# Performance work log

Hardware: AMD Instinct MI355X
Metric: run time of the kernel (lower is better)

The kernel has to match this reference:

```python
import jax, jax.numpy as jnp
import numpy as np

K = 9
BN_EPS = 1e-5
NEG_SLOPE = 0.2


def setup_inputs() -> dict:
    key = jax.random.key(0)
    ks = jax.random.split(key, 8)
    B, C, H, W = 16, 128, 32, 32
    s1 = 1.0 / np.sqrt(2 * C)
    s2 = 1.0 / np.sqrt(C)
    return {
        "x": jax.random.normal(ks[0], (B, C, H, W), dtype=jnp.float32),
        "W1": jax.random.uniform(ks[1], (2 * C, C), dtype=jnp.float32, minval=-s1, maxval=s1),
        "b1": jax.random.uniform(ks[2], (C,), dtype=jnp.float32, minval=-s1, maxval=s1),
        "W2": jax.random.uniform(ks[3], (C, C), dtype=jnp.float32, minval=-s2, maxval=s2),
        "b2": jax.random.uniform(ks[4], (C,), dtype=jnp.float32, minval=-s2, maxval=s2),
        "gamma": jnp.ones((C,), dtype=jnp.float32),
        "beta": jnp.zeros((C,), dtype=jnp.float32),
    }


def _leaky_relu(h):
    return jnp.where(h >= 0, h, NEG_SLOPE * h)


def reference(x, W1, b1, W2, b2, gamma, beta):
    B, C, H, W = x.shape
    N = H * W
    r = x
    feats = x.reshape(B, C, N).transpose(0, 2, 1)  # (B, N, C)

    # pairwise squared Euclidean distances (ordering identical to torch.cdist p=2)
    sq = jnp.sum(feats * feats, axis=-1)  # (B, N)
    d2 = sq[:, :, None] + sq[:, None, :] - 2.0 * jnp.einsum("bnc,bmc->bnm", feats, feats)
    _, idx = jax.lax.top_k(-d2, K)  # k smallest distances -> (B, N, K) int32

    neighbors = jax.vmap(lambda f, i: f[i])(feats, idx)  # (B, N, K, C)
    center = feats[:, :, None, :]  # (B, N, 1, C)
    edge = jnp.concatenate(
        [jnp.broadcast_to(center, neighbors.shape), neighbors - center], axis=-1
    )  # (B, N, K, 2C)

    h = _leaky_relu(edge @ W1 + b1)
    h = h @ W2 + b2  # (B, N, K, C)
    msg = jnp.max(h, axis=2)  # (B, N, C)

    out = msg.transpose(0, 2, 1).reshape(B, C, H, W)

    # BatchNorm2d (training mode: batch statistics, biased variance)
    mean = jnp.mean(out, axis=(0, 2, 3), keepdims=True)
    var = jnp.mean((out - mean) ** 2, axis=(0, 2, 3), keepdims=True)
    g = gamma.reshape(1, C, 1, 1)
    b = beta.reshape(1, C, 1, 1)
    out = g * (out - mean) * jax.lax.rsqrt(var + BN_EPS) + b

    return jax.nn.relu(out + r)
```

## Files before the change

### kernel.cpp

```cpp
#include <hip/hip_runtime.h>

#define B_ 16
#define C_ 128
#define N_ 1024
#define K_ 9
#define NEG_SLOPE 0.2f
#define BN_EPS 1e-5f

typedef __attribute__((ext_vector_type(8))) short short8;
typedef __attribute__((ext_vector_type(4))) float f32x4;
typedef __attribute__((ext_vector_type(4))) unsigned short u16x4;

__device__ __forceinline__ unsigned short f2bf(float f) {
    union { float f; unsigned u; } v; v.f = f;
    unsigned r = v.u + 0x7fffu + ((v.u >> 16) & 1u);
    return (unsigned short)(r >> 16);
}
__device__ __forceinline__ float bf2f(unsigned short h) {
    union { unsigned u; float f; } v; v.u = ((unsigned)h) << 16; return v.f;
}
__device__ __forceinline__ unsigned umin_(unsigned a, unsigned b) { return a < b ? a : b; }

__global__ __launch_bounds__(256) void k_stage(const float* __restrict__ x,
        const float* __restrict__ W1, const float* __restrict__ W2,
        float* __restrict__ featsT, unsigned short* __restrict__ Bf,
        float* __restrict__ sq, unsigned short* __restrict__ wf1,
        unsigned short* __restrict__ wf2)
{
    int blk = blockIdx.x;
    int tid = threadIdx.x;

    if (blk >= 512) {
        int t = (blk - 512) * 256 + tid;
        if (t < 4096) {
            int kk = t >> 9, w = (t >> 6) & 7, lane = t & 63;
            int quad = lane >> 4, col = lane & 15;
            #pragma unroll
            for (int j = 0; j < 8; ++j)
                wf1[t * 8 + j] = f2bf(W1[(kk * 32 + quad * 8 + j) * C_ + 16 * w + col]);
        } else {
            int t2 = t - 4096;
            int kk = t2 >> 9, w = (t2 >> 6) & 7, lane = t2 & 63;
            int quad = lane >> 4, col = lane & 15;
            #pragma unroll
            for (int j = 0; j < 8; ++j)
                wf2[t2 * 8 + j] = f2bf(W2[(kk * 32 + quad * 8 + j) * C_ + 16 * w + col]);
        }
        return;
    }

    __shared__ float tch[128][33];
    int b = blk >> 5;
    int n0 = (blk & 31) * 32;

    const float4* xv = (const float4*)x;
    #pragma unroll
    for (int pass = 0; pass < 4; ++pass) {
        int c = pass * 32 + (tid >> 3);
        int f = tid & 7;
        float4 v = xv[(b * C_ + c) * 256 + (n0 >> 2) + f];
        tch[c][f * 4 + 0] = v.x; tch[c][f * 4 + 1] = v.y;
        tch[c][f * 4 + 2] = v.z; tch[c][f * 4 + 3] = v.w;
    }
    __syncthreads();

    #pragma unroll
    for (int pass = 0; pass < 16; ++pass) {
        int li = pass * 256 + tid;
        int p = li >> 7, c = li & 127;
        featsT[(b * N_ + n0 + p) * C_ + c] = tch[c][p];
    }

    int lane = tid & 63, wv = tid >> 6;
    int half = lane >> 5, l2 = lane & 31;
    int ch0 = (l2 & 15) * 8;
    #pragma unroll
    for (int sub = 0; sub < 4; ++sub) {
        int pl = sub * 8 + wv * 2 + half;
        int n = n0 + pl;
        float a0 = tch[ch0 + 0][pl], a1 = tch[ch0 + 1][pl];
        float a2 = tch[ch0 + 2][pl], a3 = tch[ch0 + 3][pl];
        float a4 = tch[ch0 + 4][pl], a5 = tch[ch0 + 5][pl];
        float a6 = tch[ch0 + 6][pl], a7 = tch[ch0 + 7][pl];

        u16x4 o0, o1;
        if (l2 < 16) {
            o0.x = f2bf(a0); o0.y = f2bf(a1); o0.z = f2bf(a2); o0.w = f2bf(a3);
            o1.x = f2bf(a4); o1.y = f2bf(a5); o1.z = f2bf(a6); o1.w = f2bf(a7);
        } else {
            o0.x = f2bf(a0 - bf2f(f2bf(a0))); o0.y = f2bf(a1 - bf2f(f2bf(a1)));
            o0.z = f2bf(a2 - bf2f(f2bf(a2))); o0.w = f2bf(a3 - bf2f(f2bf(a3)));
            o1.x = f2bf(a4 - bf2f(f2bf(a4))); o1.y = f2bf(a5 - bf2f(f2bf(a5)));
            o1.z = f2bf(a6 - bf2f(f2bf(a6))); o1.w = f2bf(a7 - bf2f(f2bf(a7)));
        }
        long chunk = (((long)(b * 8 + (l2 >> 2)) * 64 + (n >> 4)) << 6)
                   + ((l2 & 3) * 16 + (n & 15));
        *(u16x4*)&Bf[chunk * 8]     = o0;
        *(u16x4*)&Bf[chunk * 8 + 4] = o1;

        float ss = a0*a0 + a1*a1 + a2*a2 + a3*a3 + a4*a4 + a5*a5 + a6*a6 + a7*a7;
        #pragma unroll
        for (int off = 1; off < 16; off <<= 1)
            ss += __shfl_xor(ss, off);
        if (l2 == 0) sq[b * N_ + n] = ss;
    }
}

#define STAGE_READ(PH, VARR) do {                                              \
    const int tl_ = (PH) >> 1, rb_ = ((PH) & 1) * 2;                           \
    _Pragma("unroll")                                                          \
    for (int t = 0; t < 8; ++t) {                                              \
        int col = ((wv * 8 + t) << 4) + cl;                                    \
        keybuf[quad * 2 + 0][col] = karr[tl_][t][rb_ + 0];                     \
        keybuf[quad * 2 + 1][col] = karr[tl_][t][rb_ + 1];                     \
    }                                                                          \
    __syncthreads();                                                           \
    _Pragma("unroll")                                                          \
    for (int j = 0; j < 16; ++j) VARR[j] = keybuf[wv][lane + (j << 6)];        \
    __syncthreads();                                                           \
} while (0)

#define TOP2_INIT(VARR, M1, M2, J1, J2) do {                                   \
    M1 = 0xFFFFFFFFu; M2 = 0xFFFFFFFFu; J1 = 0; J2 = 0;                        \
    _Pragma("unroll")                                                          \
    for (int j = 0; j < 16; ++j) {                                             \
        unsigned x_ = VARR[j], jc_ = (unsigned)j;                              \
        bool b1_ = x_ < M1, b2_ = x_ < M2;                                     \
        unsigned tk_ = b1_ ? M1 : x_, tj_ = b1_ ? J1 : jc_;                    \
        M2 = b2_ ? tk_ : M2; J2 = b2_ ? tj_ : J2;                              \
        M1 = b1_ ? x_ : M1; J1 = b1_ ? jc_ : J1;                               \
    }                                                                          \
} while (0)

#define ROW_ROUND(VARR, M1, M2, J1, J2, G, ROWPTR) do {                        \
    bool t_ = (M1 == (G));                                                     \
    unsigned long long bal_ = __ballot(t_);                                    \
    bool win_;                                                                 \
    if (__popcll(bal_) > 1) {               \
        unsigned mc_ = t_ ? (unsigned)(lane + (J1 << 6)) : 0xFFFFFFFFu;        \
        unsigned cm_ = mc_;                                                    \
        _Pragma("unroll")                                                      \
        for (int off = 1; off < 64; off <<= 1)                                 \
            cm_ = umin_(cm_, (unsigned)__shfl_xor((int)cm_, off));             \
        win_ = t_ && (mc_ == cm_);                   \
    } else {                                                                   \
        win_ = t_;                                                             \
    }                                                                          \
    if (win_) {                                                                \
        idxout[(ROWPTR) + q] = lane + (int)(J1 << 6);                          \
        unsigned gk_ = M1, gj_ = J1;                                           \
        M1 = M2; J1 = J2; M2 = 0xFFFFFFFFu;                                    \
        if (M1 == 0xFFFFFFFFu) {             \
            _Pragma("unroll")                                                  \
            for (int j = 0; j < 16; ++j) {                                     \
                unsigned x_ = VARR[j], jc_ = (unsigned)j;                      \
                bool dead_ = (x_ < gk_) || (x_ == gk_ && jc_ <= gj_);          \
                unsigned xk_ = dead_ ? 0xFFFFFFFFu : x_;                       \
                bool b1_ = xk_ < M1, b2_ = xk_ < M2;                           \
                unsigned tk_ = b1_ ? M1 : xk_, tj_ = b1_ ? J1 : jc_;           \
                M2 = b2_ ? tk_ : M2; J2 = b2_ ? tj_ : J2;                      \
                M1 = b1_ ? xk_ : M1; J1 = b1_ ? jc_ : J1;                      \
            }                                                                  \
        }                                                                      \
    }                                                                          \
} while (0)

__global__ __launch_bounds__(512, 4) void k_knn(
        const unsigned short* __restrict__ Bf, const float* __restrict__ sq,
        int* __restrict__ idxout)
{
    __shared__ unsigned keybuf[8][1028];
    __shared__ float sqn[32];

    int L = blockIdx.x;
    int xcd = L & 7, slot = L >> 3;
    int b = xcd * 2 + (slot >> 5);
    int tile32 = slot & 31;
    int n0 = tile32 * 32;
    int tid = threadIdx.x;

    if (tid < 32) sqn[tid] = sq[b * N_ + n0 + tid];
    __syncthreads();

    int wv = tid >> 6, lane = tid & 63, quad = lane >> 4, cl = lane & 15;

    f32x4 acc[2][8];
    #pragma unroll
    for (int tl = 0; tl < 2; ++tl)
        #pragma unroll
        for (int t = 0; t < 8; ++t) acc[tl][t] = (f32x4){0.f, 0.f, 0.f, 0.f};

    const short8* bfp = (const short8*)Bf;
    #pragma unroll
    for (int kb = 0; kb < 4; ++kb) {
        long ab0 = (((long)(b * 8 + kb) * 64 + tile32 * 2) << 6) + quad * 16 + cl;
        short8 afh0 = bfp[ab0];
        short8 afl0 = bfp[ab0 + 16384];
        short8 afh1 = bfp[ab0 + 64];
        short8 afl1 = bfp[ab0 + 16384 + 64];
        long bh = (((long)(b * 8 + kb) * 64 + wv * 8) << 6) + lane;
        long bl = bh + 16384;
        #pragma unroll
        for (int t = 0; t < 8; ++t) {
            short8 bfr = bfp[bh + t * 64];
            acc[0][t] = __builtin_amdgcn_mfma_f32_16x16x32_bf16(afh0, bfr, acc[0][t], 0, 0, 0);
            acc[0][t] = __builtin_amdgcn_mfma_f32_16x16x32_bf16(afl0, bfr, acc[0][t], 0, 0, 0);
            acc[1][t] = __builtin_amdgcn_mfma_f32_16x16x32_bf16(afh1, bfr, acc[1][t], 0, 0, 0);
            acc[1][t] = __builtin_amdgcn_mfma_f32_16x16x32_bf16(afl1, bfr, acc[1][t], 0, 0, 0);
        }
        #pragma unroll
        for (int t = 0; t < 8; ++t) {
            short8 bfr = bfp[bl + t * 64];
            acc[0][t] = __builtin_amdgcn_mfma_f32_16x16x32_bf16(afh0, bfr, acc[0][t], 0, 0, 0);
            acc[1][t] = __builtin_amdgcn_mfma_f32_16x16x32_bf16(afh1, bfr, acc[1][t], 0, 0, 0);
        }
    }

    float smc[8];
    #pragma unroll
    for (int t = 0; t < 8; ++t)
        smc[t] = sq[b * N_ + ((wv * 8 + t) << 4) + cl];

    unsigned karr[2][8][4];
    #pragma unroll
    for (int tl = 0; tl < 2; ++tl)
        #pragma unroll
        for (int t = 0; t < 8; ++t)
            #pragma unroll
            for (int r = 0; r < 4; ++r) {
                float d2 = fmaf(-2.f, acc[tl][t][r], smc[t] + sqn[tl * 16 + quad * 4 + r]);
                unsigned bits = __float_as_uint(d2);
                karr[tl][t][r] = bits ^ ((unsigned)((int)bits >> 31) | 0x80000000u);
            }

    unsigned vA[16], vB[16], vC[16], vD[16];
    STAGE_READ(0, vA);
    STAGE_READ(1, vB);
    STAGE_READ(2, vC);
    STAGE_READ(3, vD);

    int rbase = ((wv >> 1) << 2) + (wv & 1);
    int rowP0 = (b * N_ + n0 + rbase) * K_;
    int rowP1 = (b * N_ + n0 + rbase + 2) * K_;
    int rowP2 = (b * N_ + n0 + 16 + rbase) * K_;
    int rowP3 = (b * N_ + n0 + 16 + rbase + 2) * K_;

    unsigned mA1, mA2, jA1, jA2, mB1, mB2, jB1, jB2;
    unsigned mC1, mC2, jC1, jC2, mD1, mD2, jD1, jD2;
    TOP2_INIT(vA, mA1, mA2, jA1, jA2);
    TOP2_INIT(vB, mB1, mB2, jB1, jB2);
    TOP2_INIT(vC, mC1, mC2, jC1, jC2);
    TOP2_INIT(vD, mD1, mD2, jD1, jD2);

    #pragma unroll 1
    for (int q = 0; q < K_; ++q) {
        unsigned gA = mA1, gB = mB1, gC = mC1, gD = mD1;
        #pragma unroll
        for (int off = 1; off < 64; off <<= 1) {
            gA = umin_(gA, (unsigned)__shfl_xor((int)gA, off));
            gB = umin_(gB, (unsigned)__shfl_xor((int)gB, off));
            gC = umin_(gC, (unsigned)__shfl_xor((int)gC, off));
            gD = umin_(gD, (unsigned)__shfl_xor((int)gD, off));
        }
        ROW_ROUND(vA, mA1, mA2, jA1, jA2, gA, rowP0);
        ROW_ROUND(vB, mB1, mB2, jB1, jB2, gB, rowP1);
        ROW_ROUND(vC, mC1, mC2, jC1, jC2, gC, rowP2);
        ROW_ROUND(vD, mD1, mD2, jD1, jD2, gD, rowP3);
    }
}

__global__ __launch_bounds__(512, 6) void k_edge(const float* __restrict__ featsT,
        const int* __restrict__ idx, const unsigned short* __restrict__ wf1,
        const unsigned short* __restrict__ wf2, const float* __restrict__ b1,
        const float* __restrict__ b2, float* __restrict__ msg)
{
    __shared__ __align__(16) char smem[52224];
    unsigned short* diffs = (unsigned short*)smem;
    unsigned short* cenb  = (unsigned short*)(smem + 21760);
    unsigned short* h2b   = (unsigned short*)smem;
    unsigned short* h1    = (unsigned short*)(smem + 26112);
    unsigned short* ccb   = (unsigned short*)(smem + 47872);
    __shared__ int nb[72];

    int L = blockIdx.x;
    int xcd = L & 7, slot = L >> 3;
    int b = xcd * 2 + (slot >> 7);
    int tile = slot & 127;
    int n0 = tile * 8;
    int tid = threadIdx.x;

    if (tid < 72) nb[tid] = idx[(b * N_ + n0 + tid / 9) * K_ + tid % 9];
    __syncthreads();

    {
        int g = tid >> 6, j = tid & 63;
        int chunk = j & 31, ch = chunk << 2, half = j >> 5;
        const float4* fT4 = (const float4*)featsT;
        float4 cv = fT4[(b * N_ + n0 + g) * 32 + chunk];
        if (half == 0) {
            u16x4 cb; cb.x = f2bf(cv.x); cb.y = f2bf(cv.y);
            cb.z = f2bf(cv.z); cb.w = f2bf(cv.w);
            *(u16x4*)&cenb[g * 136 + ch] = cb;
        }
        int qb = half ? 5 : 0, qe = half ? 9 : 5;
        for (int q = qb; q < qe; ++q) {
            int e = g * 9 + q;
            float4 nv = fT4[(b * N_ + nb[e]) * 32 + chunk];
            u16x4 db;
            db.x = f2bf(nv.x - cv.x); db.y = f2bf(nv.y - cv.y);
            db.z = f2bf(nv.z - cv.z); db.w = f2bf(nv.w - cv.w);
            *(u16x4*)&diffs[e * 136 + ch] = db;
        }
    }
    __syncthreads();

    int wv = tid >> 6, lane = tid & 63;
    int quad = lane >> 4, cl = lane & 15;
    const short8* w1f = (const short8*)wf1;
    const short8* w2f = (const short8*)wf2;

    {
        float b1v = b1[16 * wv + cl];
        f32x4 a = (f32x4){b1v, b1v, b1v, b1v};
        #pragma unroll
        for (int kk = 0; kk < 4; ++kk) {
            short8 af = *(const short8*)&cenb[cl * 136 + kk * 32 + quad * 8];
            short8 bf = w1f[(kk * 8 + wv) * 64 + lane];
            a = __builtin_amdgcn_mfma_f32_16x16x32_bf16(af, bf, a, 0, 0, 0);
        }
        #pragma unroll
        for (int r = 0; r < 4; ++r)
            ccb[(quad * 4 + r) * 136 + 16 * wv + cl] = f2bf(a[r]);
    }

    {
        short8 wb[4];
        #pragma unroll
        for (int kb = 0; kb < 4; ++kb)
            wb[kb] = w1f[((kb + 4) * 8 + wv) * 64 + lane];
        #pragma unroll
        for (int t = 0; t < 5; ++t) {
            f32x4 a = (f32x4){0.f, 0.f, 0.f, 0.f};
            #pragma unroll
            for (int kb = 0; kb < 4; ++kb) {
                short8 af = *(const short8*)&diffs[(16 * t + cl) * 136 + kb * 32 + quad * 8];
                a = __builtin_amdgcn_mfma_f32_16x16x32_bf16(af, wb[kb], a, 0, 0, 0);
            }
            #pragma unroll
            for (int r = 0; r < 4; ++r) {
                int row = 16 * t + quad * 4 + r;
                int pt = row / 9; if (pt > 7) pt = 7;
                float v = a[r] + bf2f(ccb[pt * 136 + 16 * wv + cl]);
                v = (v >= 0.f) ? v : NEG_SLOPE * v;
                h1[row * 136 + 16 * wv + cl] = f2bf(v);
            }
        }
    }
    __syncthreads();

    {
        short8 wb[4];
        #pragma unroll
        for (int kb = 0; kb < 4; ++kb)
            wb[kb] = w2f[(kb * 8 + wv) * 64 + lane];
        #pragma unroll
        for (int t = 0; t < 5; ++t) {
            f32x4 a = (f32x4){0.f, 0.f, 0.f, 0.f};
            #pragma unroll
            for (int kb = 0; kb < 4; ++kb) {
                short8 af = *(const short8*)&h1[(16 * t + cl) * 136 + kb * 32 + quad * 8];
                a = __builtin_amdgcn_mfma_f32_16x16x32_bf16(af, wb[kb], a, 0, 0, 0);
            }
            #pragma unroll
            for (int r = 0; r < 4; ++r)
                h2b[(16 * t + quad * 4 + r) * 136 + 16 * wv + cl] = f2bf(a[r]);
        }
    }
    __syncthreads();

    int p = tid & 7, nb8 = tid >> 3;
    #pragma unroll
    for (int it = 0; it < 2; ++it) {
        int n = nb8 + 64 * it;
        float m = bf2f(h2b[(p * 9) * 136 + n]);
        #pragma unroll
        for (int q = 1; q < 9; ++q)
            m = fmaxf(m, bf2f(h2b[(p * 9 + q) * 136 + n]));
        msg[(b * C_ + n) * N_ + n0 + p] = m + b2[n];
    }
}

__global__ __launch_bounds__(256) void k_bnstats(const float* __restrict__ msg,
        const float* __restrict__ gamma, const float* __restrict__ beta,
        float* __restrict__ scale, float* __restrict__ shift)
{
    int c = blockIdx.x, tid = threadIdx.x;
    const float4* m4 = (const float4*)msg;
    float4 s4 = {0.f, 0.f, 0.f, 0.f}, ss4 = {0.f, 0.f, 0.f, 0.f};
    #pragma unroll
    for (int b = 0; b < B_; ++b) {
        float4 v = m4[(b * C_ + c) * 256 + tid];
        s4.x += v.x; s4.y += v.y; s4.z += v.z; s4.w += v.w;
        ss4.x += v.x * v.x; ss4.y += v.y * v.y;
        ss4.z += v.z * v.z; ss4.w += v.w * v.w;
    }
    float s = (s4.x + s4.y) + (s4.z + s4.w);
    float ss = (ss4.x + ss4.y) + (ss4.z + ss4.w);
    __shared__ float rs[256], rss[256];
    rs[tid] = s; rss[tid] = ss;
    __syncthreads();
    for (int off = 128; off > 0; off >>= 1) {
        if (tid < off) { rs[tid] += rs[tid + off]; rss[tid] += rss[tid + off]; }
        __syncthreads();
    }
    if (tid == 0) {
        float mean = rs[0] / (float)(B_ * N_);
        float var = rss[0] / (float)(B_ * N_) - mean * mean;
        float inv = 1.0f / sqrtf(var + BN_EPS);
        float g = gamma[c];
        scale[c] = g * inv;
        shift[c] = beta[c] - g * inv * mean;
    }
}

__global__ __launch_bounds__(256) void k_final(const float* __restrict__ msg,
        const float* __restrict__ x, const float* __restrict__ scale,
        const float* __restrict__ shift, float* __restrict__ out)
{
    int i = blockIdx.x * 256 + threadIdx.x;
    int e = i << 2;
    int c = (e >> 10) & 127;
    float sc = scale[c], sh = shift[c];
    float4 m4 = reinterpret_cast<const float4*>(msg)[i];
    float4 x4 = reinterpret_cast<const float4*>(x)[i];
    float4 o;
    o.x = fmaxf(m4.x * sc + sh + x4.x, 0.f);
    o.y = fmaxf(m4.y * sc + sh + x4.y, 0.f);
    o.z = fmaxf(m4.z * sc + sh + x4.z, 0.f);
    o.w = fmaxf(m4.w * sc + sh + x4.w, 0.f);
    reinterpret_cast<float4*>(out)[i] = o;
}

extern "C" void kernel_launch(void* const* d_in, const int* in_sizes, int n_in,
                              void* d_out, int out_size, void* d_ws, size_t ws_size,
                              hipStream_t stream)
{
    const float* x     = (const float*)d_in[0];
    const float* W1    = (const float*)d_in[1];
    const float* b1    = (const float*)d_in[2];
    const float* W2    = (const float*)d_in[3];
    const float* b2    = (const float*)d_in[4];
    const float* gamma = (const float*)d_in[5];
    const float* beta  = (const float*)d_in[6];
    float* out = (float*)d_out;

    float* ws     = (float*)d_ws;
    float* featsT = ws;
    float* msg    = ws + 2097152;
    unsigned short* Bf = (unsigned short*)(ws + 2097152);
    float* sq     = ws + 4194304;
    float* scale  = ws + 4210688;
    float* shift  = ws + 4210816;
    int*   idx    = (int*)(ws + 4210944);
    unsigned short* wf1 = (unsigned short*)(ws + 4358400);
    unsigned short* wf2 = (unsigned short*)(ws + 4374784);

    k_stage  <<< 536, 256, 0, stream>>>(x, W1, W2, featsT, Bf, sq, wf1, wf2);
    k_knn    <<< 512, 512, 0, stream>>>(Bf, sq, idx);
    k_edge   <<<2048, 512, 0, stream>>>(featsT, idx, wf1, wf2, b1, b2, msg);
    k_bnstats<<< 128, 256, 0, stream>>>(msg, gamma, beta, scale, shift);
    k_final  <<<2048, 256, 0, stream>>>(msg, x, scale, shift, out);
}
```

Baseline: 142.0 us.

## Halve kNN row tile to 16 and split each row's top-k across half-waves

The kNN kernel now processes 16 query rows per block instead of 32, doubling the grid to 1024 blocks. Each half-wavefront (32 lanes) owns one query row, holding 32 candidate keys per lane instead of a full wavefront handling four rows with 16 keys per lane. The change aims for more parallelism and shorter dependent shuffle chains in the selection loop, with one row per thread group instead of four interleaved rows. In exchange each block reloads the full B operand for only 16 rows, roughly doubling redundant global/L2 traffic, and register pressure per thread rises.

```diff
diff --git a/kernel.cpp b/kernel.cpp
--- a/kernel.cpp
+++ b/kernel.cpp
@@ -106,113 +106,47 @@
     }
 }
 
-#define STAGE_READ(PH, VARR) do {                                              \
-    const int tl_ = (PH) >> 1, rb_ = ((PH) & 1) * 2;                           \
-    _Pragma("unroll")                                                          \
-    for (int t = 0; t < 8; ++t) {                                              \
-        int col = ((wv * 8 + t) << 4) + cl;                                    \
-        keybuf[quad * 2 + 0][col] = karr[tl_][t][rb_ + 0];                     \
-        keybuf[quad * 2 + 1][col] = karr[tl_][t][rb_ + 1];                     \
-    }                                                                          \
-    __syncthreads();                                                           \
-    _Pragma("unroll")                                                          \
-    for (int j = 0; j < 16; ++j) VARR[j] = keybuf[wv][lane + (j << 6)];        \
-    __syncthreads();                                                           \
-} while (0)
-
-#define TOP2_INIT(VARR, M1, M2, J1, J2) do {                                   \
-    M1 = 0xFFFFFFFFu; M2 = 0xFFFFFFFFu; J1 = 0; J2 = 0;                        \
-    _Pragma("unroll")                                                          \
-    for (int j = 0; j < 16; ++j) {                                             \
-        unsigned x_ = VARR[j], jc_ = (unsigned)j;                              \
-        bool b1_ = x_ < M1, b2_ = x_ < M2;                                     \
-        unsigned tk_ = b1_ ? M1 : x_, tj_ = b1_ ? J1 : jc_;                    \
-        M2 = b2_ ? tk_ : M2; J2 = b2_ ? tj_ : J2;                              \
-        M1 = b1_ ? x_ : M1; J1 = b1_ ? jc_ : J1;                               \
-    }                                                                          \
-} while (0)
-
-#define ROW_ROUND(VARR, M1, M2, J1, J2, G, ROWPTR) do {                        \
-    bool t_ = (M1 == (G));                                                     \
-    unsigned long long bal_ = __ballot(t_);                                    \
-    bool win_;                                                                 \
-    if (__popcll(bal_) > 1) {               \
-        unsigned mc_ = t_ ? (unsigned)(lane + (J1 << 6)) : 0xFFFFFFFFu;        \
-        unsigned cm_ = mc_;                                                    \
-        _Pragma("unroll")                                                      \
-        for (int off = 1; off < 64; off <<= 1)                                 \
-            cm_ = umin_(cm_, (unsigned)__shfl_xor((int)cm_, off));             \
-        win_ = t_ && (mc_ == cm_);                   \
-    } else {                                                                   \
-        win_ = t_;                                                             \
-    }                                                                          \
-    if (win_) {                                                                \
-        idxout[(ROWPTR) + q] = lane + (int)(J1 << 6);                          \
-        unsigned gk_ = M1, gj_ = J1;                                           \
-        M1 = M2; J1 = J2; M2 = 0xFFFFFFFFu;                                    \
-        if (M1 == 0xFFFFFFFFu) {             \
-            _Pragma("unroll")                                                  \
-            for (int j = 0; j < 16; ++j) {                                     \
-                unsigned x_ = VARR[j], jc_ = (unsigned)j;                      \
-                bool dead_ = (x_ < gk_) || (x_ == gk_ && jc_ <= gj_);          \
-                unsigned xk_ = dead_ ? 0xFFFFFFFFu : x_;                       \
-                bool b1_ = xk_ < M1, b2_ = xk_ < M2;                           \
-                unsigned tk_ = b1_ ? M1 : xk_, tj_ = b1_ ? J1 : jc_;           \
-                M2 = b2_ ? tk_ : M2; J2 = b2_ ? tj_ : J2;                      \
-                M1 = b1_ ? xk_ : M1; J1 = b1_ ? jc_ : J1;                      \
-            }                                                                  \
-        }                                                                      \
-    }                                                                          \
-} while (0)
-
 __global__ __launch_bounds__(512, 4) void k_knn(
         const unsigned short* __restrict__ Bf, const float* __restrict__ sq,
         int* __restrict__ idxout)
 {
-    __shared__ unsigned keybuf[8][1028];
-    __shared__ float sqn[32];
+    __shared__ unsigned keybuf[8][1032];
+    __shared__ float sqn[16];
 
     int L = blockIdx.x;
     int xcd = L & 7, slot = L >> 3;
-    int b = xcd * 2 + (slot >> 5);
-    int tile32 = slot & 31;
-    int n0 = tile32 * 32;
+    int b = xcd * 2 + (slot >> 6);
+    int tile = slot & 63;
+    int n0 = tile * 16;
     int tid = threadIdx.x;
 
-    if (tid < 32) sqn[tid] = sq[b * N_ + n0 + tid];
+    if (tid < 16) sqn[tid] = sq[b * N_ + n0 + tid];
     __syncthreads();
 
     int wv = tid >> 6, lane = tid & 63, quad = lane >> 4, cl = lane & 15;
 
-    f32x4 acc[2][8];
-    #pragma unroll
-    for (int tl = 0; tl < 2; ++tl)
-        #pragma unroll
-        for (int t = 0; t < 8; ++t) acc[tl][t] = (f32x4){0.f, 0.f, 0.f, 0.f};
+    f32x4 acc[8];
+    #pragma unroll
+    for (int t = 0; t < 8; ++t) acc[t] = (f32x4){0.f, 0.f, 0.f, 0.f};
 
     const short8* bfp = (const short8*)Bf;
     #pragma unroll
     for (int kb = 0; kb < 4; ++kb) {
-        long ab0 = (((long)(b * 8 + kb) * 64 + tile32 * 2) << 6) + quad * 16 + cl;
-        short8 afh0 = bfp[ab0];
-        short8 afl0 = bfp[ab0 + 16384];
-        short8 afh1 = bfp[ab0 + 64];
-        short8 afl1 = bfp[ab0 + 16384 + 64];
+        long abase = (((long)(b * 8 + kb) * 64 + tile) << 6) + quad * 16 + cl;
+        short8 afh = bfp[abase];
+        short8 afl = bfp[abase + 16384];
         long bh = (((long)(b * 8 + kb) * 64 + wv * 8) << 6) + lane;
         long bl = bh + 16384;
         #pragma unroll
         for (int t = 0; t < 8; ++t) {
             short8 bfr = bfp[bh + t * 64];
-            acc[0][t] = __builtin_amdgcn_mfma_f32_16x16x32_bf16(afh0, bfr, acc[0][t], 0, 0, 0);
-            acc[0][t] = __builtin_amdgcn_mfma_f32_16x16x32_bf16(afl0, bfr, acc[0][t], 0, 0, 0);
-            acc[1][t] = __builtin_amdgcn_mfma_f32_16x16x32_bf16(afh1, bfr, acc[1][t], 0, 0, 0);
-            acc[1][t] = __builtin_amdgcn_mfma_f32_16x16x32_bf16(afl1, bfr, acc[1][t], 0, 0, 0);
+            acc[t] = __builtin_amdgcn_mfma_f32_16x16x32_bf16(afh, bfr, acc[t], 0, 0, 0);
+            acc[t] = __builtin_amdgcn_mfma_f32_16x16x32_bf16(afl, bfr, acc[t], 0, 0, 0);
         }
         #pragma unroll
         for (int t = 0; t < 8; ++t) {
             short8 bfr = bfp[bl + t * 64];
-            acc[0][t] = __builtin_amdgcn_mfma_f32_16x16x32_bf16(afh0, bfr, acc[0][t], 0, 0, 0);
-            acc[1][t] = __builtin_amdgcn_mfma_f32_16x16x32_bf16(afh1, bfr, acc[1][t], 0, 0, 0);
+            acc[t] = __builtin_amdgcn_mfma_f32_16x16x32_bf16(afh, bfr, acc[t], 0, 0, 0);
         }
     }
 
@@ -221,51 +155,88 @@
     for (int t = 0; t < 8; ++t)
         smc[t] = sq[b * N_ + ((wv * 8 + t) << 4) + cl];
 
-    unsigned karr[2][8][4];
-    #pragma unroll
-    for (int tl = 0; tl < 2; ++tl)
-        #pragma unroll
-        for (int t = 0; t < 8; ++t)
-            #pragma unroll
-            for (int r = 0; r < 4; ++r) {
-                float d2 = fmaf(-2.f, acc[tl][t][r], smc[t] + sqn[tl * 16 + quad * 4 + r]);
-                unsigned bits = __float_as_uint(d2);
-                karr[tl][t][r] = bits ^ ((unsigned)((int)bits >> 31) | 0x80000000u);
-            }
-
-    unsigned vA[16], vB[16], vC[16], vD[16];
-    STAGE_READ(0, vA);
-    STAGE_READ(1, vB);
-    STAGE_READ(2, vC);
-    STAGE_READ(3, vD);
-
-    int rbase = ((wv >> 1) << 2) + (wv & 1);
-    int rowP0 = (b * N_ + n0 + rbase) * K_;
-    int rowP1 = (b * N_ + n0 + rbase + 2) * K_;
-    int rowP2 = (b * N_ + n0 + 16 + rbase) * K_;
-    int rowP3 = (b * N_ + n0 + 16 + rbase + 2) * K_;
-
-    unsigned mA1, mA2, jA1, jA2, mB1, mB2, jB1, jB2;
-    unsigned mC1, mC2, jC1, jC2, mD1, mD2, jD1, jD2;
-    TOP2_INIT(vA, mA1, mA2, jA1, jA2);
-    TOP2_INIT(vB, mB1, mB2, jB1, jB2);
-    TOP2_INIT(vC, mC1, mC2, jC1, jC2);
-    TOP2_INIT(vD, mD1, mD2, jD1, jD2);
+    unsigned karr[8][4];
+    #pragma unroll
+    for (int t = 0; t < 8; ++t)
+        #pragma unroll
+        for (int r = 0; r < 4; ++r) {
+            float d2 = fmaf(-2.f, acc[t][r], smc[t] + sqn[quad * 4 + r]);
+            unsigned bits = __float_as_uint(d2);
+            karr[t][r] = bits ^ ((unsigned)((int)bits >> 31) | 0x80000000u);
+        }
+
+    int grp = lane >> 5, l32 = lane & 31;
+    int myphase = wv >> 2;
+    int kr_r = ((wv & 3) << 1) + grp;
+    unsigned v[32];
+    #pragma unroll
+    for (int ph = 0; ph < 2; ++ph) {
+        #pragma unroll
+        for (int t = 0; t < 8; ++t) {
+            int col = ((wv * 8 + t) << 4) + cl;
+            keybuf[quad * 2 + 0][col] = karr[t][ph * 2 + 0];
+            keybuf[quad * 2 + 1][col] = karr[t][ph * 2 + 1];
+        }
+        __syncthreads();
+        if (myphase == ph) {
+            #pragma unroll
+            for (int j = 0; j < 32; ++j)
+                v[j] = keybuf[kr_r][(j << 5) + l32];
+        }
+        __syncthreads();
+    }
+
+    int rowq = ((kr_r >> 1) << 2) + (myphase << 1) + (kr_r & 1);
+    long orow = (long)(b * N_ + n0 + rowq) * K_;
+
+    unsigned m1 = 0xFFFFFFFFu, m2 = 0xFFFFFFFFu, j1 = 0, j2 = 0;
+    #pragma unroll
+    for (int j = 0; j < 32; ++j) {
+        unsigned x_ = v[j], jc = (unsigned)j;
+        bool b1 = x_ < m1, b2 = x_ < m2;
+        unsigned tk = b1 ? m1 : x_, tj = b1 ? j1 : jc;
+        m2 = b2 ? tk : m2; j2 = b2 ? tj : j2;
+        m1 = b1 ? x_ : m1; j1 = b1 ? jc : j1;
+    }
 
     #pragma unroll 1
     for (int q = 0; q < K_; ++q) {
-        unsigned gA = mA1, gB = mB1, gC = mC1, gD = mD1;
-        #pragma unroll
-        for (int off = 1; off < 64; off <<= 1) {
-            gA = umin_(gA, (unsigned)__shfl_xor((int)gA, off));
-            gB = umin_(gB, (unsigned)__shfl_xor((int)gB, off));
-            gC = umin_(gC, (unsigned)__shfl_xor((int)gC, off));
-            gD = umin_(gD, (unsigned)__shfl_xor((int)gD, off));
-        }
-        ROW_ROUND(vA, mA1, mA2, jA1, jA2, gA, rowP0);
-        ROW_ROUND(vB, mB1, mB2, jB1, jB2, gB, rowP1);
-        ROW_ROUND(vC, mC1, mC2, jC1, jC2, gC, rowP2);
-        ROW_ROUND(vD, mD1, mD2, jD1, jD2, gD, rowP3);
+        unsigned g = m1;
+        #pragma unroll
+        for (int off = 1; off < 32; off <<= 1)
+            g = umin_(g, (unsigned)__shfl_xor((int)g, off));
+
+        bool tied = (m1 == g);
+        unsigned long long bal = __ballot(tied);
+        unsigned balg = (unsigned)(bal >> (grp << 5));
+        bool win;
+        if (__popc(balg) > 1) {
+            unsigned mc = tied ? ((j1 << 5) + (unsigned)l32) : 0xFFFFFFFFu;
+            unsigned cm = mc;
+            #pragma unroll
+            for (int off = 1; off < 32; off <<= 1)
+                cm = umin_(cm, (unsigned)__shfl_xor((int)cm, off));
+            win = tied && (mc == cm);
+        } else {
+            win = tied;
+        }
+        if (win) {
+            idxout[orow + q] = (int)((j1 << 5) + (unsigned)l32);
+            unsigned gk = m1, gj = j1;
+            m1 = m2; j1 = j2; m2 = 0xFFFFFFFFu;
+            if (m1 == 0xFFFFFFFFu) {
+                #pragma unroll
+                for (int j = 0; j < 32; ++j) {
+                    unsigned x_ = v[j], jc = (unsigned)j;
+                    bool dead = (x_ < gk) || (x_ == gk && jc <= gj);
+                    unsigned xk = dead ? 0xFFFFFFFFu : x_;
+                    bool b1 = xk < m1, b2 = xk < m2;
+                    unsigned tk = b1 ? m1 : xk, tj = b1 ? j1 : jc;
+                    m2 = b2 ? tk : m2; j2 = b2 ? tj : j2;
+                    m1 = b1 ? xk : m1; j1 = b1 ? jc : j1;
+                }
+            }
+        }
     }
 }
 
@@ -466,7 +437,7 @@
     unsigned short* wf2 = (unsigned short*)(ws + 4374784);
 
     k_stage  <<< 536, 256, 0, stream>>>(x, W1, W2, featsT, Bf, sq, wf1, wf2);
-    k_knn    <<< 512, 512, 0, stream>>>(Bf, sq, idx);
+    k_knn    <<<1024, 512, 0, stream>>>(Bf, sq, idx);
     k_edge   <<<2048, 512, 0, stream>>>(featsT, idx, wf1, wf2, b1, b2, msg);
     k_bnstats<<< 128, 256, 0, stream>>>(msg, gamma, beta, scale, shift);
     k_final  <<<2048, 256, 0, stream>>>(msg, x, scale, shift, out);
```

After: 153.7 us. 8.3% more time.
